# Optimization experiments

Measured on AMD Instinct MI355X. Metric: run time of the kernel, lower is better.

The kernel has to match this reference:

```python
import jax, jax.numpy as jnp
import numpy as np

N_AGENTS = 32
STATE_DIM = 512
LATENT = 16
H = 64  # attention_hidden_dim
N1 = N_AGENTS
N2 = N_AGENTS * (N_AGENTS - 1) // 2
NF = N1 + N2
B = 32768
# pairwise indices, same order as itertools.combinations(range(n), 2)
_PI, _PJ = np.triu_indices(N_AGENTS, k=1)
PI = jnp.asarray(_PI)
PJ = jnp.asarray(_PJ)


def setup_inputs() -> dict:
    key = jax.random.key(0)
    ks = jax.random.split(key, 24)
    s = 0.1  # small init scale (xavier gain 0.5)
    inp = {
        "agent_q_values": jax.random.normal(ks[0], (B, N_AGENTS), jnp.float32),
        "state": jax.random.normal(ks[1], (B, STATE_DIM), jnp.float32),
        "agent_semantics": jax.random.normal(ks[2], (B, N_AGENTS, LATENT), jnp.float32),
        # order-1 shape functions, stacked over N1 functions, weights in [in,out] layout
        "w1_1": jax.random.normal(ks[3], (N1, 1, 8), jnp.float32) * s,
        "b1_1": jnp.zeros((N1, 8), jnp.float32),
        "w2_1": jax.random.normal(ks[4], (N1, 8, 4), jnp.float32) * s,
        "b2_1": jnp.zeros((N1, 4), jnp.float32),
        "w3_1": jax.random.normal(ks[5], (N1, 4, 1), jnp.float32) * s,
        "b3_1": jnp.zeros((N1, 1), jnp.float32),
        # order-2 shape functions, stacked over N2 pairs
        "w1_2": jax.random.normal(ks[6], (N2, 2, 8), jnp.float32) * s,
        "b1_2": jnp.zeros((N2, 8), jnp.float32),
        "w2_2": jax.random.normal(ks[7], (N2, 8, 4), jnp.float32) * s,
        "b2_2": jnp.zeros((N2, 4), jnp.float32),
        "w3_2": jax.random.normal(ks[8], (N2, 4, 1), jnp.float32) * s,
        "b3_2": jnp.zeros((N2, 1), jnp.float32),
        # state encoder
        "ws_w": jax.random.normal(ks[9], (STATE_DIM, H), jnp.float32) * (1.0 / np.sqrt(STATE_DIM)),
        "ws_b": jnp.zeros((H,), jnp.float32),
        # semantic encoder
        "wz_w": jax.random.normal(ks[10], (LATENT * N_AGENTS, H), jnp.float32) * (1.0 / np.sqrt(LATENT * N_AGENTS)),
        "wz_b": jnp.zeros((H,), jnp.float32),
        # attention net
        "wa1_w": jax.random.normal(ks[11], (2 * H, H), jnp.float32) * (1.0 / np.sqrt(2 * H)),
        "wa1_b": jnp.zeros((H,), jnp.float32),
        "wa2_w": jax.random.normal(ks[12], (H, NF), jnp.float32) * (1.0 / np.sqrt(H)),
        "wa2_b": jnp.zeros((NF,), jnp.float32),
        # bias net
        "wb1_w": jax.random.normal(ks[13], (STATE_DIM, H), jnp.float32) * (1.0 / np.sqrt(STATE_DIM)),
        "wb1_b": jnp.zeros((H,), jnp.float32),
        "wb2_w": jax.random.normal(ks[14], (H, 1), jnp.float32) * (1.0 / np.sqrt(H)),
        "wb2_b": jnp.zeros((1,), jnp.float32),
    }
    return inp


def _shape_fns(x, w1, b1, w2, b2, w3, b3):
    # x: [B, N, D_in]; weights stacked over N functions; abs() on weights (monotonicity)
    h = jax.nn.elu(jnp.einsum("bnd,ndh->bnh", x, jnp.abs(w1)) + b1)   # [B,N,8]
    h = jax.nn.elu(jnp.einsum("bnh,nhk->bnk", h, jnp.abs(w2)) + b2)   # [B,N,4]
    f = jnp.einsum("bnk,nk->bn", h, jnp.abs(w3)[:, :, 0]) + b3[:, 0]  # [B,N]
    return f


def reference(agent_q_values, state, agent_semantics,
              w1_1, b1_1, w2_1, b2_1, w3_1, b3_1,
              w1_2, b1_2, w2_2, b2_2, w3_2, b3_2,
              ws_w, ws_b, wz_w, wz_b,
              wa1_w, wa1_b, wa2_w, wa2_b,
              wb1_w, wb1_b, wb2_w, wb2_b):
    q = agent_q_values  # [B, n_agents]
    # order-1 shape functions: input is scalar Q_i
    f1 = _shape_fns(q[:, :, None], w1_1, b1_1, w2_1, b2_1, w3_1, b3_1)   # [B, N1]
    # order-2 shape functions: input is [Q_i, Q_j] per pair
    q_pairs = jnp.stack([q[:, PI], q[:, PJ]], axis=-1)                    # [B, N2, 2]
    f2 = _shape_fns(q_pairs, w1_2, b1_2, w2_2, b2_2, w3_2, b3_2)          # [B, N2]
    shape_outputs = jnp.concatenate([f1, f2], axis=-1)                    # [B, NF]

    state_enc = jax.nn.relu(state @ ws_w + ws_b)                          # [B, H]
    sem_flat = agent_semantics.reshape(agent_semantics.shape[0], -1)      # [B, n*latent]
    sem_enc = jax.nn.relu(sem_flat @ wz_w + wz_b)                         # [B, H]
    combined = jnp.concatenate([state_enc, sem_enc], axis=-1)             # [B, 2H]
    logits = jax.nn.relu(combined @ wa1_w + wa1_b) @ wa2_w + wa2_b        # [B, NF]
    attention_weights = jax.nn.softmax(logits, axis=-1)

    weighted_sum = jnp.sum(attention_weights * shape_outputs, axis=-1, keepdims=True)
    bias = jax.nn.relu(state @ wb1_w + wb1_b) @ wb2_w + wb2_b             # [B, 1]
    q_total = weighted_sum + bias
    return (q_total, attention_weights, shape_outputs)
```

## Files before the change

kernel.cpp:

```cpp
#include <hip/hip_runtime.h>
#include <cstdint>
#include <cstddef>

#define NAG 32
#define N1C 32
#define N2C 496
#define NF 528
#define HD 64
#define SD 512

typedef __attribute__((ext_vector_type(8))) short bf16x8;
typedef __attribute__((ext_vector_type(4))) float f32x4;
#define MFMA16(a, b, c) __builtin_amdgcn_mfma_f32_16x16x32_bf16(a, b, c, 0, 0, 0)

__device__ __forceinline__ unsigned short f2bf(float f) {
    unsigned int u = __float_as_uint(f);
    u += 0x7fffu + ((u >> 16) & 1u);
    return (unsigned short)(u >> 16);
}
__device__ __forceinline__ unsigned int pack2(float a, float b) {
    return (unsigned int)f2bf(a) | ((unsigned int)f2bf(b) << 16);
}
__device__ __forceinline__ float elu_f(float x) {
    return x > 0.f ? x : (__expf(x) - 1.f);
}

#define OFF_WST   0
#define OFF_WB1T  32768
#define OFF_WZT   65536
#define OFF_WA1T  98304
#define OFF_WA2T  106496
#define PREP_TOT  140288

__global__ __launch_bounds__(256) void prep_kernel(
    const float* __restrict__ ws_w, const float* __restrict__ wb1_w,
    const float* __restrict__ wz_w, const float* __restrict__ wa1_w,
    const float* __restrict__ wa2_w, unsigned short* __restrict__ ws)
{
    int i = blockIdx.x * 256 + threadIdx.x;
    if (i >= PREP_TOT) return;
    float v;
    if (i < OFF_WA1T) {
        int region = i >> 15;
        int j = i & 32767;
        int e = j & 7, lane = (j >> 3) & 63, ct = (j >> 9) & 3, ks = j >> 11;
        int n = ct * 16 + (lane & 15);
        int k = ks * 32 + (lane >> 4) * 8 + e;
        const float* src = region == 0 ? ws_w : (region == 1 ? wb1_w : wz_w);
        v = src[k * 64 + n];
    } else if (i < OFF_WA2T) {
        int j = i - OFF_WA1T;
        int e = j & 7, lane = (j >> 3) & 63, ct = (j >> 9) & 3, ks = j >> 11;
        int n = ct * 16 + (lane & 15);
        int k = ks * 32 + (lane >> 4) * 8 + e;
        v = wa1_w[k * 64 + n];
    } else {
        int j = i - OFF_WA2T;
        int e = j & 7, lane = (j >> 3) & 63, hh = (j >> 9) & 1, nt = j >> 10;
        int n = nt * 16 + (lane & 15);
        int k = hh * 32 + (lane >> 4) * 8 + e;
        v = wa2_w[k * NF + n];
    }
    ws[i] = f2bf(v);
}

#define SROWS 64
__global__ __launch_bounds__(576) void shape_kernel(
    const float* __restrict__ q,
    const float* __restrict__ w1_1, const float* __restrict__ b1_1,
    const float* __restrict__ w2_1, const float* __restrict__ b2_1,
    const float* __restrict__ w3_1, const float* __restrict__ b3_1,
    const float* __restrict__ w1_2, const float* __restrict__ b1_2,
    const float* __restrict__ w2_2, const float* __restrict__ b2_2,
    const float* __restrict__ w3_2, const float* __restrict__ b3_2,
    float* __restrict__ shape_out, int B)
{
    __shared__ float qs[SROWS][NAG];

    int tid = threadIdx.x;
    int f = tid;
    bool valid = f < NF;
    int fe = valid ? f : (NF - 1);

    float w1a[8], w1b[8], b1v[8], w2v[32], b2v[4], w3v[4], b3v;
    int pi, pj;
    if (fe < N1C) {
        int n = fe;
        pi = n; pj = n;
        #pragma unroll
        for (int k = 0; k < 8; k++) { w1a[k] = fabsf(w1_1[n*8+k]); w1b[k] = 0.f; b1v[k] = b1_1[n*8+k]; }
        #pragma unroll
        for (int t = 0; t < 32; t++) w2v[t] = fabsf(w2_1[n*32+t]);
        #pragma unroll
        for (int j = 0; j < 4; j++) { b2v[j] = b2_1[n*4+j]; w3v[j] = fabsf(w3_1[n*4+j]); }
        b3v = b3_1[n];
    } else {
        int n = fe - N1C;
        int p = n, i = 0, c = NAG - 1;
        while (p >= c) { p -= c; c--; i++; }
        pi = i; pj = i + 1 + p;
        #pragma unroll
        for (int k = 0; k < 8; k++) { w1a[k] = fabsf(w1_2[n*16+k]); w1b[k] = fabsf(w1_2[n*16+8+k]); b1v[k] = b1_2[n*8+k]; }
        #pragma unroll
        for (int t = 0; t < 32; t++) w2v[t] = fabsf(w2_2[n*32+t]);
        #pragma unroll
        for (int j = 0; j < 4; j++) { b2v[j] = b2_2[n*4+j]; w3v[j] = fabsf(w3_2[n*4+j]); }
        b3v = b3_2[n];
    }

    int row0 = blockIdx.x * SROWS;
    if (tid < 512) {
        float4 v = *(const float4*)&q[(size_t)row0 * NAG + tid * 4];
        *(float4*)&((float*)qs)[tid * 4] = v;
    }
    __syncthreads();

    #pragma unroll 4
    for (int rr = 0; rr < SROWS; rr++) {
        float qi = qs[rr][pi];
        float qj = qs[rr][pj];
        float h1[8];
        #pragma unroll
        for (int k = 0; k < 8; k++) h1[k] = elu_f(w1a[k]*qi + w1b[k]*qj + b1v[k]);
        float h2[4];
        #pragma unroll
        for (int j = 0; j < 4; j++) {
            float a = b2v[j];
            #pragma unroll
            for (int k = 0; k < 8; k++) a += h1[k] * w2v[k*4 + j];
            h2[j] = elu_f(a);
        }
        float fv = b3v;
        #pragma unroll
        for (int j = 0; j < 4; j++) fv += h2[j] * w3v[j];
        if (valid) shape_out[(size_t)(row0 + rr) * NF + f] = fv;
    }
}

#define RB 64
#define KH 256
#define SAP 264

__global__ __launch_bounds__(256, 2) void enc_mfma(
    const float* __restrict__ state,
    const float* __restrict__ sem,
    const unsigned short* __restrict__ wsbuf,
    const float* __restrict__ ws_b, const float* __restrict__ wz_b,
    const float* __restrict__ wa1_b, const float* __restrict__ wa2_b,
    const float* __restrict__ wb1_b, const float* __restrict__ wb2_w,
    const float* __restrict__ wb2_b,
    const float* __restrict__ shape_out,
    float* __restrict__ q_total,
    float* __restrict__ attn_out)
{
    __shared__ unsigned short sA[RB][SAP];
    __shared__ unsigned short sComb[RB][136];
    __shared__ unsigned short sH[RB][72];

    int tid  = threadIdx.x;
    int lane = tid & 63;
    int w    = tid >> 6;
    int col  = lane & 15;
    int quad = lane >> 4;
    int r0   = blockIdx.x * RB;
    int rowt = w * 16;

    const unsigned short* fS  = wsbuf + OFF_WST  + lane * 8;
    const unsigned short* fB  = wsbuf + OFF_WB1T + lane * 8;
    const unsigned short* fZ  = wsbuf + OFF_WZT  + lane * 8;
    const unsigned short* fA1 = wsbuf + OFF_WA1T + lane * 8;
    const unsigned short* fA2 = wsbuf + OFF_WA2T + lane * 8;

    f32x4 accS[4], accB[4], accZ[4];
    #pragma unroll
    for (int ct = 0; ct < 4; ct++) {
        accS[ct] = (f32x4){0.f,0.f,0.f,0.f};
        accB[ct] = (f32x4){0.f,0.f,0.f,0.f};
        accZ[ct] = (f32x4){0.f,0.f,0.f,0.f};
    }

    #pragma unroll 1
    for (int h = 0; h < 2; h++) {
        int c0 = h * KH;
        #pragma unroll
        for (int b = 0; b < 2; b++) {
            float4 v[8];
            #pragma unroll
            for (int i = 0; i < 8; i++)
                v[i] = *(const float4*)&state[(size_t)(r0 + rowt + b*8 + i) * SD + c0 + lane * 4];
            #pragma unroll
            for (int i = 0; i < 8; i++) {
                uint2 p; p.x = pack2(v[i].x, v[i].y); p.y = pack2(v[i].z, v[i].w);
                *(uint2*)&sA[rowt + b*8 + i][lane * 4] = p;
            }
        }
        #pragma unroll
        for (int ks = 0; ks < 8; ks++) {
            bf16x8 a = *(const bf16x8*)&sA[rowt + col][ks * 32 + quad * 8];
            int fof = (h * 8 + ks) * 4 * 512;
            #pragma unroll
            for (int ct = 0; ct < 4; ct++) {
                bf16x8 bS = *(const bf16x8*)(fS + fof + ct * 512);
                bf16x8 bB = *(const bf16x8*)(fB + fof + ct * 512);
                accS[ct] = MFMA16(a, bS, accS[ct]);
                accB[ct] = MFMA16(a, bB, accB[ct]);
            }
        }
    }

    #pragma unroll 1
    for (int h = 0; h < 2; h++) {
        int c0 = h * KH;
        #pragma unroll
        for (int b = 0; b < 2; b++) {
            float4 v[8];
            #pragma unroll
            for (int i = 0; i < 8; i++)
                v[i] = *(const float4*)&sem[(size_t)(r0 + rowt + b*8 + i) * SD + c0 + lane * 4];
            #pragma unroll
            for (int i = 0; i < 8; i++) {
                uint2 p; p.x = pack2(v[i].x, v[i].y); p.y = pack2(v[i].z, v[i].w);
                *(uint2*)&sA[rowt + b*8 + i][lane * 4] = p;
            }
        }
        #pragma unroll
        for (int ks = 0; ks < 8; ks++) {
            bf16x8 a = *(const bf16x8*)&sA[rowt + col][ks * 32 + quad * 8];
            int fof = (h * 8 + ks) * 4 * 512;
            #pragma unroll
            for (int ct = 0; ct < 4; ct++) {
                bf16x8 bZ = *(const bf16x8*)(fZ + fof + ct * 512);
                accZ[ct] = MFMA16(a, bZ, accZ[ct]);
            }
        }
    }

    #pragma unroll
    for (int ct = 0; ct < 4; ct++) {
        float bs = ws_b[ct * 16 + col];
        float bz = wz_b[ct * 16 + col];
        #pragma unroll
        for (int reg = 0; reg < 4; reg++) {
            int rr = rowt + quad * 4 + reg;
            sComb[rr][ct * 16 + col]      = f2bf(fmaxf(accS[ct][reg] + bs, 0.f));
            sComb[rr][64 + ct * 16 + col] = f2bf(fmaxf(accZ[ct][reg] + bz, 0.f));
        }
    }

    float qbv[4];
    #pragma unroll
    for (int reg = 0; reg < 4; reg++) {
        float p = 0.f;
        #pragma unroll
        for (int ct = 0; ct < 4; ct++)
            p += fmaxf(accB[ct][reg] + wb1_b[ct * 16 + col], 0.f) * wb2_w[ct * 16 + col];
        #pragma unroll
        for (int m = 1; m < 16; m <<= 1) p += __shfl_xor(p, m, 64);
        qbv[reg] = p;
    }

    f32x4 accH[4];
    #pragma unroll
    for (int ct = 0; ct < 4; ct++) accH[ct] = (f32x4){0.f,0.f,0.f,0.f};
    #pragma unroll
    for (int ks = 0; ks < 4; ks++) {
        bf16x8 a = *(const bf16x8*)&sComb[rowt + col][ks * 32 + quad * 8];
        #pragma unroll
        for (int ct = 0; ct < 4; ct++) {
            bf16x8 b = *(const bf16x8*)(fA1 + (ks * 4 + ct) * 512);
            accH[ct] = MFMA16(a, b, accH[ct]);
        }
    }
    #pragma unroll
    for (int ct = 0; ct < 4; ct++) {
        float bh = wa1_b[ct * 16 + col];
        #pragma unroll
        for (int reg = 0; reg < 4; reg++)
            sH[rowt + quad * 4 + reg][ct * 16 + col] = f2bf(fmaxf(accH[ct][reg] + bh, 0.f));
    }

    bf16x8 ha0 = *(const bf16x8*)&sH[rowt + col][quad * 8];
    bf16x8 ha1 = *(const bf16x8*)&sH[rowt + col][32 + quad * 8];

    float sAcc[4] = {0.f,0.f,0.f,0.f};
    float wAcc[4] = {0.f,0.f,0.f,0.f};
    for (int nt = 0; nt < 33; nt++) {
        f32x4 acc = (f32x4){0.f,0.f,0.f,0.f};
        acc = MFMA16(ha0, *(const bf16x8*)(fA2 + nt * 1024), acc);
        acc = MFMA16(ha1, *(const bf16x8*)(fA2 + nt * 1024 + 512), acc);
        float lb = wa2_b[nt * 16 + col];
        #pragma unroll
        for (int reg = 0; reg < 4; reg++) {
            float e = __expf(acc[reg] + lb);
            sAcc[reg] += e;
            wAcc[reg] += e * shape_out[(size_t)(r0 + rowt + quad * 4 + reg) * NF + nt * 16 + col];
        }
    }
    float inv[4];
    #pragma unroll
    for (int reg = 0; reg < 4; reg++) {
        float s = sAcc[reg], ww = wAcc[reg];
        #pragma unroll
        for (int m = 1; m < 16; m <<= 1) { s += __shfl_xor(s, m, 64); ww += __shfl_xor(ww, m, 64); }
        inv[reg] = 1.f / s;
        if (col == 0)
            q_total[r0 + rowt + quad * 4 + reg] = ww * inv[reg] + qbv[reg] + wb2_b[0];
    }

    for (int nt = 0; nt < 33; nt++) {
        f32x4 acc = (f32x4){0.f,0.f,0.f,0.f};
        acc = MFMA16(ha0, *(const bf16x8*)(fA2 + nt * 1024), acc);
        acc = MFMA16(ha1, *(const bf16x8*)(fA2 + nt * 1024 + 512), acc);
        float lb = wa2_b[nt * 16 + col];
        #pragma unroll
        for (int reg = 0; reg < 4; reg++) {
            float e = __expf(acc[reg] + lb);
            attn_out[(size_t)(r0 + rowt + quad * 4 + reg) * NF + nt * 16 + col] = e * inv[reg];
        }
    }
}

extern "C" void kernel_launch(void* const* d_in, const int* in_sizes, int n_in,
                              void* d_out, int out_size, void* d_ws, size_t ws_size,
                              hipStream_t stream) {
    const float* q     = (const float*)d_in[0];
    const float* state = (const float*)d_in[1];
    const float* sem   = (const float*)d_in[2];
    const float* w1_1  = (const float*)d_in[3];
    const float* b1_1  = (const float*)d_in[4];
    const float* w2_1  = (const float*)d_in[5];
    const float* b2_1  = (const float*)d_in[6];
    const float* w3_1  = (const float*)d_in[7];
    const float* b3_1  = (const float*)d_in[8];
    const float* w1_2  = (const float*)d_in[9];
    const float* b1_2  = (const float*)d_in[10];
    const float* w2_2  = (const float*)d_in[11];
    const float* b2_2  = (const float*)d_in[12];
    const float* w3_2  = (const float*)d_in[13];
    const float* b3_2  = (const float*)d_in[14];
    const float* ws_w  = (const float*)d_in[15];
    const float* ws_b  = (const float*)d_in[16];
    const float* wz_w  = (const float*)d_in[17];
    const float* wz_b  = (const float*)d_in[18];
    const float* wa1_w = (const float*)d_in[19];
    const float* wa1_b = (const float*)d_in[20];
    const float* wa2_w = (const float*)d_in[21];
    const float* wa2_b = (const float*)d_in[22];
    const float* wb1_w = (const float*)d_in[23];
    const float* wb1_b = (const float*)d_in[24];
    const float* wb2_w = (const float*)d_in[25];
    const float* wb2_b = (const float*)d_in[26];

    int B = in_sizes[0] / NAG;

    float* out_q    = (float*)d_out;
    float* out_attn = out_q + B;
    float* out_shp  = out_attn + (size_t)B * NF;

    unsigned short* wsbuf = (unsigned short*)d_ws;

    prep_kernel<<<(PREP_TOT + 255) / 256, 256, 0, stream>>>(
        ws_w, wb1_w, wz_w, wa1_w, wa2_w, wsbuf);

    shape_kernel<<<B / SROWS, 576, 0, stream>>>(q,
        w1_1, b1_1, w2_1, b2_1, w3_1, b3_1,
        w1_2, b1_2, w2_2, b2_2, w3_2, b3_2,
        out_shp, B);

    enc_mfma<<<B / RB, 256, 0, stream>>>(state, sem, wsbuf,
        ws_b, wz_b, wa1_b, wa2_b, wb1_b, wb2_w, wb2_b,
        out_shp, out_q, out_attn);
}
```

Before: 374.3 us.

## Fuse shape-function computation into the encoder/attention MFMA kernel

Removes the separate shape_kernel and computes the per-feature shape-function MLPs at the start of enc_mfma for the block's 64 rows, writing shape_out before the attention phase. The goal is to drop a kernel launch and let the later weighted-sum read shape outputs that were just written, likely still in cache. The cost is that 256 threads now cover 528 features in three passes with heavy per-thread weight registers, under a launch bound of two blocks per SM. That may raise register pressure and serialize ALU-heavy work ahead of the MFMA stage.

New measurement: 373.8 us. About the same (-0.1%).

```diff
diff --git a/kernel.cpp b/kernel.cpp
--- a/kernel.cpp
+++ b/kernel.cpp
@@ -64,84 +64,12 @@
     ws[i] = f2bf(v);
 }
 
-#define SROWS 64
-__global__ __launch_bounds__(576) void shape_kernel(
-    const float* __restrict__ q,
-    const float* __restrict__ w1_1, const float* __restrict__ b1_1,
-    const float* __restrict__ w2_1, const float* __restrict__ b2_1,
-    const float* __restrict__ w3_1, const float* __restrict__ b3_1,
-    const float* __restrict__ w1_2, const float* __restrict__ b1_2,
-    const float* __restrict__ w2_2, const float* __restrict__ b2_2,
-    const float* __restrict__ w3_2, const float* __restrict__ b3_2,
-    float* __restrict__ shape_out, int B)
-{
-    __shared__ float qs[SROWS][NAG];
-
-    int tid = threadIdx.x;
-    int f = tid;
-    bool valid = f < NF;
-    int fe = valid ? f : (NF - 1);
-
-    float w1a[8], w1b[8], b1v[8], w2v[32], b2v[4], w3v[4], b3v;
-    int pi, pj;
-    if (fe < N1C) {
-        int n = fe;
-        pi = n; pj = n;
-        #pragma unroll
-        for (int k = 0; k < 8; k++) { w1a[k] = fabsf(w1_1[n*8+k]); w1b[k] = 0.f; b1v[k] = b1_1[n*8+k]; }
-        #pragma unroll
-        for (int t = 0; t < 32; t++) w2v[t] = fabsf(w2_1[n*32+t]);
-        #pragma unroll
-        for (int j = 0; j < 4; j++) { b2v[j] = b2_1[n*4+j]; w3v[j] = fabsf(w3_1[n*4+j]); }
-        b3v = b3_1[n];
-    } else {
-        int n = fe - N1C;
-        int p = n, i = 0, c = NAG - 1;
-        while (p >= c) { p -= c; c--; i++; }
-        pi = i; pj = i + 1 + p;
-        #pragma unroll
-        for (int k = 0; k < 8; k++) { w1a[k] = fabsf(w1_2[n*16+k]); w1b[k] = fabsf(w1_2[n*16+8+k]); b1v[k] = b1_2[n*8+k]; }
-        #pragma unroll
-        for (int t = 0; t < 32; t++) w2v[t] = fabsf(w2_2[n*32+t]);
-        #pragma unroll
-        for (int j = 0; j < 4; j++) { b2v[j] = b2_2[n*4+j]; w3v[j] = fabsf(w3_2[n*4+j]); }
-        b3v = b3_2[n];
-    }
-
-    int row0 = blockIdx.x * SROWS;
-    if (tid < 512) {
-        float4 v = *(const float4*)&q[(size_t)row0 * NAG + tid * 4];
-        *(float4*)&((float*)qs)[tid * 4] = v;
-    }
-    __syncthreads();
-
-    #pragma unroll 4
-    for (int rr = 0; rr < SROWS; rr++) {
-        float qi = qs[rr][pi];
-        float qj = qs[rr][pj];
-        float h1[8];
-        #pragma unroll
-        for (int k = 0; k < 8; k++) h1[k] = elu_f(w1a[k]*qi + w1b[k]*qj + b1v[k]);
-        float h2[4];
-        #pragma unroll
-        for (int j = 0; j < 4; j++) {
-            float a = b2v[j];
-            #pragma unroll
-            for (int k = 0; k < 8; k++) a += h1[k] * w2v[k*4 + j];
-            h2[j] = elu_f(a);
-        }
-        float fv = b3v;
-        #pragma unroll
-        for (int j = 0; j < 4; j++) fv += h2[j] * w3v[j];
-        if (valid) shape_out[(size_t)(row0 + rr) * NF + f] = fv;
-    }
-}
-
 #define RB 64
 #define KH 256
 #define SAP 264
 
 __global__ __launch_bounds__(256, 2) void enc_mfma(
+    const float* __restrict__ q,
     const float* __restrict__ state,
     const float* __restrict__ sem,
     const unsigned short* __restrict__ wsbuf,
@@ -149,13 +77,20 @@
     const float* __restrict__ wa1_b, const float* __restrict__ wa2_b,
     const float* __restrict__ wb1_b, const float* __restrict__ wb2_w,
     const float* __restrict__ wb2_b,
-    const float* __restrict__ shape_out,
+    const float* __restrict__ w1_1, const float* __restrict__ b1_1,
+    const float* __restrict__ w2_1, const float* __restrict__ b2_1,
+    const float* __restrict__ w3_1, const float* __restrict__ b3_1,
+    const float* __restrict__ w1_2, const float* __restrict__ b1_2,
+    const float* __restrict__ w2_2, const float* __restrict__ b2_2,
+    const float* __restrict__ w3_2, const float* __restrict__ b3_2,
+    float* __restrict__ shape_out,
     float* __restrict__ q_total,
     float* __restrict__ attn_out)
 {
     __shared__ unsigned short sA[RB][SAP];
     __shared__ unsigned short sComb[RB][136];
     __shared__ unsigned short sH[RB][72];
+    __shared__ float qs[RB][36];
 
     int tid  = threadIdx.x;
     int lane = tid & 63;
@@ -164,6 +99,69 @@
     int quad = lane >> 4;
     int r0   = blockIdx.x * RB;
     int rowt = w * 16;
+
+    {
+        int idx = tid * 8;
+        int qr  = idx >> 5;
+        int qc  = idx & 31;
+        float4 v0 = *(const float4*)&q[(size_t)(r0 + qr) * NAG + qc];
+        float4 v1 = *(const float4*)&q[(size_t)(r0 + qr) * NAG + qc + 4];
+        qs[qr][qc + 0] = v0.x; qs[qr][qc + 1] = v0.y;
+        qs[qr][qc + 2] = v0.z; qs[qr][qc + 3] = v0.w;
+        qs[qr][qc + 4] = v1.x; qs[qr][qc + 5] = v1.y;
+        qs[qr][qc + 6] = v1.z; qs[qr][qc + 7] = v1.w;
+    }
+    __syncthreads();
+
+    for (int fi = 0; fi < 3; fi++) {
+        int f = tid + fi * 256;
+        if (f >= NF) break;
+        float w1a[8], w1b[8], b1v[8], w2v[32], b2v[4], w3v[4], b3v;
+        int pi, pj;
+        if (f < N1C) {
+            int n = f; pi = n; pj = n;
+            #pragma unroll
+            for (int k = 0; k < 8; k++) { w1a[k] = fabsf(w1_1[n*8+k]); w1b[k] = 0.f; b1v[k] = b1_1[n*8+k]; }
+            #pragma unroll
+            for (int t = 0; t < 32; t++) w2v[t] = fabsf(w2_1[n*32+t]);
+            #pragma unroll
+            for (int j = 0; j < 4; j++) { b2v[j] = b2_1[n*4+j]; w3v[j] = fabsf(w3_1[n*4+j]); }
+            b3v = b3_1[n];
+        } else {
+            int n = f - N1C;
+            int p = n, ii = 0, c = NAG - 1;
+            while (p >= c) { p -= c; c--; ii++; }
+            pi = ii; pj = ii + 1 + p;
+            #pragma unroll
+            for (int k = 0; k < 8; k++) { w1a[k] = fabsf(w1_2[n*16+k]); w1b[k] = fabsf(w1_2[n*16+8+k]); b1v[k] = b1_2[n*8+k]; }
+            #pragma unroll
+            for (int t = 0; t < 32; t++) w2v[t] = fabsf(w2_2[n*32+t]);
+            #pragma unroll
+            for (int j = 0; j < 4; j++) { b2v[j] = b2_2[n*4+j]; w3v[j] = fabsf(w3_2[n*4+j]); }
+            b3v = b3_2[n];
+        }
+        #pragma unroll 4
+        for (int rr = 0; rr < RB; rr++) {
+            float qi = qs[rr][pi];
+            float qj = qs[rr][pj];
+            float h1[8];
+            #pragma unroll
+            for (int k = 0; k < 8; k++) h1[k] = elu_f(w1a[k]*qi + w1b[k]*qj + b1v[k]);
+            float h2[4];
+            #pragma unroll
+            for (int j = 0; j < 4; j++) {
+                float a = b2v[j];
+                #pragma unroll
+                for (int k = 0; k < 8; k++) a += h1[k] * w2v[k*4 + j];
+                h2[j] = elu_f(a);
+            }
+            float fv = b3v;
+            #pragma unroll
+            for (int j = 0; j < 4; j++) fv += h2[j] * w3v[j];
+            shape_out[(size_t)(r0 + rr) * NF + f] = fv;
+        }
+    }
+    __syncthreads();
 
     const unsigned short* fS  = wsbuf + OFF_WST  + lane * 8;
     const unsigned short* fB  = wsbuf + OFF_WB1T + lane * 8;
@@ -362,12 +360,9 @@
     prep_kernel<<<(PREP_TOT + 255) / 256, 256, 0, stream>>>(
         ws_w, wb1_w, wz_w, wa1_w, wa2_w, wsbuf);
 
-    shape_kernel<<<B / SROWS, 576, 0, stream>>>(q,
+    enc_mfma<<<B / RB, 256, 0, stream>>>(q, state, sem, wsbuf,
+        ws_b, wz_b, wa1_b, wa2_b, wb1_b, wb2_w, wb2_b,
         w1_1, b1_1, w2_1, b2_1, w3_1, b3_1,
         w1_2, b1_2, w2_2, b2_2, w3_2, b3_2,
-        out_shp, B);
-
-    enc_mfma<<<B / RB, 256, 0, stream>>>(state, sem, wsbuf,
-        ws_b, wz_b, wa1_b, wa2_b, wb1_b, wb2_w, wb2_b,
         out_shp, out_q, out_attn);
 }
```
